# Performance work log

Measured on AMD Instinct MI355X. Metric: run time of the kernel, lower is better.

The kernel has to match this reference:

```python
import jax, jax.numpy as jnp
import numpy as np

B, C, OC, H, W = 2, 64, 128, 96, 96
HD, DI, N, R, K = C // 2, C, 16, 2, 4  # VSSBlock: hidden=C/2, d_inner=2*hidden=C, d_state, dt_rank, 4 scan dirs
EPS = 1e-5


def _conv(x, w, b, pad, groups=1):
    y = jax.lax.conv_general_dilated(x, w, (1, 1), pad, feature_group_count=groups,
                                     dimension_numbers=('NCHW', 'OIHW', 'NCHW'))
    return y + b[None, :, None, None]


def _ln(x, w, b):
    m = x.mean(-1, keepdims=True)
    v = x.var(-1, keepdims=True)
    return (x - m) * jax.lax.rsqrt(v + EPS) * w + b


def _selective_scan(xs, dts, Bs, Cs, A, D):
    # xs, dts: (B,K,DI,L); Bs, Cs: (B,K,N,L); A: (K,DI,N); D: (K,DI)
    dts = jax.nn.softplus(dts)

    def step(h, inp):
        u_t, dt_t, B_t, C_t = inp
        dA = jnp.exp(dt_t[..., None] * A)                         # (B,K,DI,N)
        h = dA * h + (dt_t * u_t)[..., None] * B_t[:, :, None, :]
        return h, jnp.einsum('bkdn,bkn->bkd', h, C_t)

    seq = (jnp.moveaxis(xs, -1, 0), jnp.moveaxis(dts, -1, 0),
           jnp.moveaxis(Bs, -1, 0), jnp.moveaxis(Cs, -1, 0))
    h0 = jnp.zeros(xs.shape[:3] + (A.shape[-1],), xs.dtype)
    _, ys = jax.lax.scan(step, h0, seq)
    return jnp.moveaxis(ys, 0, -1) + D[None, :, :, None] * xs


def _vss_block(x, ln_w, ln_b, in_w, conv_w, conv_b, xproj_w, dtproj_w, dtproj_b,
               A_logs, Ds, on_w, on_b, out_w):
    # x: (B,H,W,HD); VMamba SS2D with 4-direction cross-scan + residual
    b, hh, ww, _ = x.shape
    L = hh * ww
    h = _ln(x, ln_w, ln_b)
    xz = h @ in_w                                   # (B,H,W,2*DI)
    xp, z = jnp.split(xz, 2, axis=-1)
    xc = jnp.transpose(xp, (0, 3, 1, 2))            # (B,DI,H,W)
    xc = jax.nn.silu(_conv(xc, conv_w, conv_b, ((1, 1), (1, 1)), groups=DI))
    x_flat = xc.reshape(b, DI, L)
    x_wh = jnp.transpose(xc, (0, 1, 3, 2)).reshape(b, DI, L)
    x2 = jnp.stack([x_flat, x_wh], axis=1)
    xs = jnp.concatenate([x2, jnp.flip(x2, -1)], axis=1)      # (B,4,DI,L)
    x_dbl = jnp.einsum('bkdl,kcd->bkcl', xs, xproj_w)
    dts, Bs, Cs = jnp.split(x_dbl, [R, R + N], axis=2)
    dts = jnp.einsum('bkrl,kdr->bkdl', dts, dtproj_w) + dtproj_b[None, :, :, None]
    A = -jnp.exp(A_logs)
    ys = _selective_scan(xs, dts, Bs, Cs, A, Ds)              # (B,4,DI,L)
    inv = jnp.flip(ys[:, 2:4], -1)
    unwh = lambda t: jnp.transpose(t.reshape(b, DI, ww, hh), (0, 1, 3, 2)).reshape(b, DI, L)
    y = ys[:, 0] + inv[:, 0] + unwh(ys[:, 1]) + unwh(inv[:, 1])
    y = jnp.transpose(y.reshape(b, DI, hh, ww), (0, 2, 3, 1))
    y = _ln(y, on_w, on_b) * jax.nn.silu(z)
    return x + y @ out_w


def _forward(x, ms_dw33_w, ms_dw33_b, ms_in_w, ms_in_b, ms_scale,
             vss_ln_w, vss_ln_b, vss_in_w, vss_conv_w, vss_conv_b, vss_xproj_w,
             vss_dtproj_w, vss_dtproj_b, vss_A_logs, vss_Ds, vss_on_w, vss_on_b, vss_out_w,
             ma_conv_w, ma_conv_b, adw_h_w, adw_h_b, adw_w_w, adw_w_b,
             pw_w, pw_b, bn_w, bn_b, bn_mean, bn_var):
    vss = (vss_ln_w, vss_ln_b, vss_in_w, vss_conv_w, vss_conv_b, vss_xproj_w,
           vss_dtproj_w, vss_dtproj_b, vss_A_logs, vss_Ds, vss_on_w, vss_on_b, vss_out_w)
    # --- MambaSplit (shared VSSBlock applied to both channel halves) ---
    xd = _conv(x, ms_dw33_w, ms_dw33_b, ((1, 1), (1, 1)), groups=C)
    x1, x2 = jnp.split(xd, 2, axis=1)

    def branch(xp):
        y = _vss_block(jnp.transpose(xp, (0, 2, 3, 1)), *vss)
        return ms_scale * xp + jnp.transpose(y, (0, 3, 1, 2))

    xm = jnp.concatenate([branch(x1), branch(x2)], axis=1)
    m = xm.mean((2, 3), keepdims=True)
    v = xm.var((2, 3), keepdims=True)
    xm = (xm - m) * jax.lax.rsqrt(v + EPS) * ms_in_w[None, :, None, None] + ms_in_b[None, :, None, None]
    xm = jax.nn.leaky_relu(xm, 0.01)
    # --- MaxAvg (global avg+max pool -> 3x3 conv on 1x1 map -> sigmoid gate) ---
    pooled = jnp.concatenate([x.mean((2, 3), keepdims=True), x.max((2, 3), keepdims=True)], axis=1)
    gate = jax.nn.sigmoid(_conv(pooled, ma_conv_w, ma_conv_b, ((1, 1), (1, 1))))
    xs_ = xm + gate * x
    # --- AxialDW ---
    xs_ = xs_ + _conv(xs_, adw_h_w, adw_h_b, ((1, 1), (0, 0)), groups=C) \
              + _conv(xs_, adw_w_w, adw_w_b, ((0, 0), (1, 1)), groups=C)
    # --- BN (eval) + ReLU, 1x1 conv, 2x2 maxpool ---
    skip = jax.nn.relu((xs_ - bn_mean[None, :, None, None]) * jax.lax.rsqrt(bn_var[None, :, None, None] + EPS)
                       * bn_w[None, :, None, None] + bn_b[None, :, None, None])
    out = _conv(skip, pw_w, pw_b, ((0, 0), (0, 0)))
    down = jax.lax.reduce_window(out, -jnp.inf, jax.lax.max, (1, 1, 2, 2), (1, 1, 2, 2), 'VALID')
    return down, skip


def setup_inputs() -> dict:
    key = jax.random.key(0)
    ks = jax.random.split(key, 16)
    r = lambda i, shape, s=0.02: jax.random.normal(ks[i], shape, jnp.float32) * s
    return {
        'x': jax.random.normal(ks[0], (B, C, H, W), jnp.float32),
        'ms_dw33_w': r(1, (C, 1, 3, 3), 0.1), 'ms_dw33_b': jnp.zeros(C),
        'ms_in_w': jnp.ones(C), 'ms_in_b': jnp.zeros(C),
        'ms_scale': jnp.ones((1,)),
        'vss_ln_w': jnp.ones(HD), 'vss_ln_b': jnp.zeros(HD),
        'vss_in_w': r(2, (HD, 2 * DI)),
        'vss_conv_w': r(3, (DI, 1, 3, 3), 0.1), 'vss_conv_b': jnp.zeros(DI),
        'vss_xproj_w': r(4, (K, R + 2 * N, DI)),
        'vss_dtproj_w': r(5, (K, DI, R), 0.1), 'vss_dtproj_b': r(6, (K, DI), 0.1),
        'vss_A_logs': jnp.tile(jnp.log(jnp.arange(1, N + 1, dtype=jnp.float32)), (K, DI, 1)),
        'vss_Ds': jnp.ones((K, DI)),
        'vss_on_w': jnp.ones(DI), 'vss_on_b': jnp.zeros(DI),
        'vss_out_w': r(7, (DI, HD)),
        'ma_conv_w': r(8, (C, 2 * C, 3, 3), 0.05), 'ma_conv_b': jnp.zeros(C),
        'adw_h_w': r(9, (C, 1, 3, 1), 0.1), 'adw_h_b': jnp.zeros(C),
        'adw_w_w': r(10, (C, 1, 1, 3), 0.1), 'adw_w_b': jnp.zeros(C),
        'pw_w': r(11, (OC, C, 1, 1)), 'pw_b': jnp.zeros(OC),
        'bn_w': jnp.ones(C), 'bn_b': jnp.zeros(C),
        'bn_mean': jnp.zeros(C), 'bn_var': jnp.ones(C),
    }


def reference(x, ms_dw33_w, ms_dw33_b, ms_in_w, ms_in_b, ms_scale,
              vss_ln_w, vss_ln_b, vss_in_w, vss_conv_w, vss_conv_b, vss_xproj_w,
              vss_dtproj_w, vss_dtproj_b, vss_A_logs, vss_Ds, vss_on_w, vss_on_b, vss_out_w,
              ma_conv_w, ma_conv_b, adw_h_w, adw_h_b, adw_w_w, adw_w_b,
              pw_w, pw_b, bn_w, bn_b, bn_mean, bn_var):
    return _forward(x, ms_dw33_w, ms_dw33_b, ms_in_w, ms_in_b, ms_scale,
                    vss_ln_w, vss_ln_b, vss_in_w, vss_conv_w, vss_conv_b, vss_xproj_w,
                    vss_dtproj_w, vss_dtproj_b, vss_A_logs, vss_Ds, vss_on_w, vss_on_b, vss_out_w,
                    ma_conv_w, ma_conv_b, adw_h_w, adw_h_b, adw_w_w, adw_w_b,
                    pw_w, pw_b, bn_w, bn_b, bn_mean, bn_var)
```

## Files before the change

kernel.cpp:

```cpp
#include <hip/hip_runtime.h>
#include <hip/hip_bf16.h>

typedef __hip_bfloat16 bf16;
#define DEV __device__ __forceinline__

constexpr int B_ = 2, C_ = 64, H_ = 96, W_ = 96, L_ = 9216;
constexpr int HD_ = 32, DI_ = 64, N_ = 16, K_ = 4, BB_ = 4;
constexpr int OC_ = 128;
constexpr int CH_ = 384, CL_ = 24;
constexpr int SEGN = 32, SEGC = 12;
constexpr int BROW = 20;
constexpr float EPSF = 1e-5f;
constexpr int DOWN_SZ = B_ * OC_ * 48 * 48;

typedef __attribute__((ext_vector_type(8))) short short8;
typedef __attribute__((ext_vector_type(4))) float f32x4;
typedef __attribute__((ext_vector_type(2))) float f32x2;

DEV float softplusf(float x) { return x > 15.f ? x : __logf(1.f + __expf(x)); }
DEV float b2f(bf16 v) { return __bfloat162float(v); }
DEV float lo16f(unsigned v) { return __uint_as_float(v << 16); }
DEV float hi16f(unsigned v) { return __uint_as_float(v & 0xffff0000u); }
DEV f32x2 pk2(unsigned w) { f32x2 r = {lo16f(w), hi16f(w)}; return r; }
DEV f32x2 lo2(f32x4 q) { f32x2 r = {q.x, q.y}; return r; }
DEV f32x2 hi2(f32x4 q) { f32x2 r = {q.z, q.w}; return r; }
DEV unsigned pkbf(float a, float b) {
  __hip_bfloat162 t;
  t.x = __float2bfloat16(a);
  t.y = __float2bfloat16(b);
  return *reinterpret_cast<unsigned*>(&t);
}
DEV void unpk8(uint4 a, float* v) {
  v[0] = lo16f(a.x); v[1] = hi16f(a.x); v[2] = lo16f(a.y); v[3] = hi16f(a.y);
  v[4] = lo16f(a.z); v[5] = hi16f(a.z); v[6] = lo16f(a.w); v[7] = hi16f(a.w);
}
DEV void unpk(uint4 a, uint4 b, float* v) {
  unpk8(a, v); unpk8(b, v + 8);
}

__constant__ float kLogN[16] = {
  0.0f, 0.69314718f, 1.09861229f, 1.38629436f, 1.60943791f, 1.79175947f,
  1.94591015f, 2.07944154f, 2.19722458f, 2.30258509f, 2.39789527f,
  2.48490665f, 2.56494936f, 2.63905733f, 2.70805020f, 2.77258872f};

DEV void pow_tree2(float e1, f32x2* ep) {
  float e2 = e1 * e1;
  ep[0].x = e1; ep[0].y = e2;
  f32x2 b2v = {e2, e2};
  ep[1] = ep[0] * b2v;
  float e4 = ep[1].y;
  f32x2 b4v = {e4, e4};
  ep[2] = ep[0] * b4v;
  ep[3] = ep[1] * b4v;
  float e8 = ep[3].y;
  f32x2 b8v = {e8, e8};
  ep[4] = ep[0] * b8v;
  ep[5] = ep[1] * b8v;
  ep[6] = ep[2] * b8v;
  ep[7] = ep[3] * b8v;
}

__global__ __launch_bounds__(256, 4) void k_front(
    const float* __restrict__ x, const float* __restrict__ dw33w,
    const float* __restrict__ dw33b, const float* __restrict__ lnw,
    const float* __restrict__ lnb, const float* __restrict__ inw,
    const float* __restrict__ xpw, const float* __restrict__ alog,
    float* __restrict__ xd, bf16* __restrict__ xzAh, bf16* __restrict__ xzBh,
    bf16* __restrict__ wh, float* __restrict__ aux) {
  int bb = blockIdx.y, t = threadIdx.x;
  int b = bb & 1, co = (bb >> 1) * HD_;
  int idx0 = blockIdx.x * 32;
  if (bb == 0) {
    int i = blockIdx.x * 256 + t;
    if (i < 144 * 64) {
      int n = i >> 6;
      wh[i] = __float2bfloat16(n < 136 ? xpw[i] : 0.f);
    }
    if (blockIdx.x == 0) {
      int kd = t;
      const float* al = alog + kd * N_;
      float a0 = al[0];
      bool lin = true;
#pragma unroll
      for (int n = 1; n < N_; n++) lin = lin && (fabsf(al[n] - a0 - kLogN[n]) < 3e-5f);
      aux[kd] = -__expf(a0);
      aux[256 + kd] = lin ? 1.f : 0.f;
#pragma unroll
      for (int n = 0; n < N_; n++) aux[512 + kd * N_ + n] = -__expf(al[n]);
    }
  }
  __shared__ float xds[32 * 36];
  __shared__ float meanA[32], rstdA[32];
  for (int i = t; i < 1024; i += 256) {
    int cl = i >> 5, ii = i & 31;
    int sp = idx0 + ii, wi = sp % 96, hi = sp / 96;
    int cg = b * C_ + co + cl;
    float acc = dw33b[co + cl];
#pragma unroll
    for (int dy = -1; dy <= 1; dy++) {
      int hh = hi + dy; if (hh < 0 || hh >= H_) continue;
#pragma unroll
      for (int dx = -1; dx <= 1; dx++) {
        int ww = wi + dx; if (ww < 0 || ww >= W_) continue;
        acc = fmaf(x[(size_t)cg * L_ + sp + dy * 96 + dx],
                   dw33w[(co + cl) * 9 + (dy + 1) * 3 + (dx + 1)], acc);
      }
    }
    xds[cl * 36 + ii] = acc;
    xd[(size_t)cg * L_ + sp] = acc;
  }
  __syncthreads();
  if (t < 32) {
    float s = 0.f, sq = 0.f;
#pragma unroll
    for (int c = 0; c < 32; c++) { float v = xds[c * 36 + t]; s += v; sq = fmaf(v, v, sq); }
    float mean = s * (1.f / HD_);
    float var = sq * (1.f / HD_) - mean * mean;
    meanA[t] = mean; rstdA[t] = rsqrtf(var + EPSF);
  }
  __syncthreads();
  for (int i = t; i < 1024; i += 256) {
    int c = i >> 5, idx = i & 31;
    float v = xds[c * 36 + idx];
    xds[c * 36 + idx] = (v - meanA[idx]) * rstdA[idx] * lnw[c] + lnb[c];
  }
  __syncthreads();
  int oc = t & 127, g = t >> 7;
  float acc[16];
#pragma unroll
  for (int j = 0; j < 16; j++) acc[j] = 0.f;
  for (int c = 0; c < 32; c++) {
    float wv = inw[c * 128 + oc];
    const float4* row = reinterpret_cast<const float4*>(&xds[c * 36 + g * 16]);
#pragma unroll
    for (int j4 = 0; j4 < 4; j4++) {
      float4 xv = row[j4];
      acc[j4 * 4 + 0] = fmaf(xv.x, wv, acc[j4 * 4 + 0]);
      acc[j4 * 4 + 1] = fmaf(xv.y, wv, acc[j4 * 4 + 1]);
      acc[j4 * 4 + 2] = fmaf(xv.z, wv, acc[j4 * 4 + 2]);
      acc[j4 * 4 + 3] = fmaf(xv.w, wv, acc[j4 * 4 + 3]);
    }
  }
  int occ = oc & 63;
  if (oc < 64) {
#pragma unroll
    for (int j = 0; j < 16; j++)
      xzAh[(size_t)(bb * L_ + idx0 + g * 16 + j) * 64 + occ] = __float2bfloat16(acc[j]);
  } else {
#pragma unroll
    for (int j = 0; j < 16; j++)
      xzBh[(size_t)(bb * L_ + idx0 + g * 16 + j) * 64 + occ] = __float2bfloat16(acc[j]);
  }
}

__global__ void k_dwsilu(const bf16* __restrict__ xzAh, const float* __restrict__ cw,
                         const float* __restrict__ cb, bf16* __restrict__ xch,
                         bf16* __restrict__ xcht) {
  int t = blockIdx.x * 256 + threadIdx.x;
  int dp = t & 31, idx = (t >> 5) % L_, bb = t / (L_ * 32);
  int d0 = dp * 2;
  int wi = idx % W_, hi = idx / W_;
  const unsigned* src = (const unsigned*)xzAh;
  float acc0 = cb[d0], acc1 = cb[d0 + 1];
#pragma unroll
  for (int dy = -1; dy <= 1; dy++) {
    int hh = hi + dy; if (hh < 0 || hh >= H_) continue;
#pragma unroll
    for (int dx = -1; dx <= 1; dx++) {
      int ww = wi + dx; if (ww < 0 || ww >= W_) continue;
      unsigned v = src[(size_t)(bb * L_ + hh * W_ + ww) * 32 + dp];
      float w0 = cw[d0 * 9 + (dy + 1) * 3 + (dx + 1)];
      float w1 = cw[(d0 + 1) * 9 + (dy + 1) * 3 + (dx + 1)];
      acc0 = fmaf(lo16f(v), w0, acc0);
      acc1 = fmaf(hi16f(v), w1, acc1);
    }
  }
  acc0 = acc0 / (1.f + __expf(-acc0));
  acc1 = acc1 / (1.f + __expf(-acc1));
  unsigned out = pkbf(acc0, acc1);
  ((unsigned*)xch)[t] = out;
  int idx_t = wi * 96 + hi;
  ((unsigned*)xcht)[((size_t)bb * L_ + idx_t) * 32 + dp] = out;
}

__global__ __launch_bounds__(256, 4) void k_xdbl_mfma(
    const bf16* __restrict__ xch, const bf16* __restrict__ wh,
    float* __restrict__ xdblB, float* __restrict__ xdblC) {
  int w = threadIdx.x >> 6, lane = threadIdx.x & 63;
  int bb = blockIdx.y;
  int mtile = blockIdx.x * 4 + w;
  int idx0 = mtile * 16;
  int m = lane & 15, quad = lane >> 4;
  const bf16* arow = xch + ((size_t)bb * L_ + idx0 + m) * 64 + quad * 8;
  short8 a0 = *reinterpret_cast<const short8*>(arow);
  short8 a1 = *reinterpret_cast<const short8*>(arow + 32);
  int ntb = blockIdx.z * 3;
#pragma unroll
  for (int it = 0; it < 3; it++) {
    int nt = ntb + it;
    int n = nt * 16 + m;
    const bf16* brow = wh + n * 64 + quad * 8;
    short8 b0 = *reinterpret_cast<const short8*>(brow);
    short8 b1 = *reinterpret_cast<const short8*>(brow + 32);
    f32x4 acc = {0.f, 0.f, 0.f, 0.f};
    acc = __builtin_amdgcn_mfma_f32_16x16x32_bf16(a0, b0, acc, 0, 0, 0);
    acc = __builtin_amdgcn_mfma_f32_16x16x32_bf16(a1, b1, acc, 0, 0, 0);
    if (n < 136) {
      int k4 = (n >= 102) ? 3 : (n >= 68) ? 2 : (n >= 34) ? 1 : 0;
      int c = n - k4 * 34;
#pragma unroll
      for (int i = 0; i < 4; i++) {
        int r = idx0 + quad * 4 + i;
        int hi2 = r / 96, wi2 = r - hi2 * 96;
        int tr = wi2 * 96 + hi2;
        int ls = (k4 == 0) ? r : (k4 == 1) ? tr : (k4 == 2) ? (L_ - 1 - r) : (L_ - 1 - tr);
        size_t row = (size_t)(bb * K_ + k4) * L_ + ls;
        if (c < 2)       xdblB[row * BROW + 16 + c] = acc[i];
        else if (c < 18) xdblB[row * BROW + (c - 2)] = acc[i];
        else             xdblC[row * 16 + (c - 18)] = acc[i];
      }
    }
  }
}

__global__ __launch_bounds__(256, 4) void k_scan1(
    const float* __restrict__ xdblB, const bf16* __restrict__ xch,
    const bf16* __restrict__ xcht, const float* __restrict__ dtw,
    const float* __restrict__ dtb, const float* __restrict__ aux,
    bf16* __restrict__ hbuf, float* __restrict__ ssum) {
  int w = threadIdx.x >> 6, d = threadIdx.x & 63;
  int bx = blockIdx.x;
  int chunk = bx * 4 + w, k = blockIdx.y, bb = blockIdx.z;
  const float* bB = xdblB + (size_t)(bb * K_ + k) * L_ * BROW;
  __shared__ __align__(16) float sB[96 * BROW];
  {
    const uint4* src = (const uint4*)(bB + (size_t)bx * 96 * BROW);
    uint4* dst = (uint4*)sB;
    for (int i = threadIdx.x; i < 480; i += 256) dst[i] = src[i];
  }
  __syncthreads();
  float w0 = dtw[(k * DI_ + d) * 2 + 0], w1 = dtw[(k * DI_ + d) * 2 + 1];
  float bia = dtb[k * DI_ + d];
  float A1 = aux[k * 64 + d];
  bool chain = (__ballot(aux[256 + k * 64 + d] > 0.5f) == ~0ull);
  const bf16* ub = ((k & 1) ? xcht : xch) + (size_t)bb * L_ * DI_;
  int ls0 = chunk * CL_;
  int uidx0 = (k & 2) ? (L_ - 1 - ls0) : ls0;
  int ustep = (k & 2) ? -1 : 1;
  float S = 0.f;
  size_t base = (size_t)((bb * K_ + k) * CH_ + chunk) * DI_ + d;
  if (chain) {
    float uv[CL_];
    const bf16* up = ub + (size_t)uidx0 * DI_ + d;
#pragma unroll
    for (int s = 0; s < CL_; s++) uv[s] = b2f(up[s * ustep * DI_]);
    f32x2 h2[8];
#pragma unroll
    for (int i = 0; i < 8; i++) { h2[i].x = 0.f; h2[i].y = 0.f; }
#pragma unroll
    for (int s = 0; s < CL_; s++) {
      const float* p = sB + (w * CL_ + s) * BROW;
      f32x4 q0 = *(const f32x4*)p;
      f32x4 q1 = *(const f32x4*)(p + 4);
      f32x4 q2 = *(const f32x4*)(p + 8);
      f32x4 q3 = *(const f32x4*)(p + 12);
      f32x2 tt = *(const f32x2*)(p + 16);
      float dt = softplusf(fmaf(tt.x, w0, fmaf(tt.y, w1, bia)));
      S += dt;
      float du = dt * uv[s];
      f32x2 du2 = {du, du};
      f32x2 ep2[8];
      pow_tree2(__expf(dt * A1), ep2);
      h2[0] = ep2[0] * h2[0] + du2 * lo2(q0);
      h2[1] = ep2[1] * h2[1] + du2 * hi2(q0);
      h2[2] = ep2[2] * h2[2] + du2 * lo2(q1);
      h2[3] = ep2[3] * h2[3] + du2 * hi2(q1);
      h2[4] = ep2[4] * h2[4] + du2 * lo2(q2);
      h2[5] = ep2[5] * h2[5] + du2 * hi2(q2);
      h2[6] = ep2[6] * h2[6] + du2 * lo2(q3);
      h2[7] = ep2[7] * h2[7] + du2 * hi2(q3);
    }
    uint4 o0, o1;
    o0.x = pkbf(h2[0].x, h2[0].y); o0.y = pkbf(h2[1].x, h2[1].y);
    o0.z = pkbf(h2[2].x, h2[2].y); o0.w = pkbf(h2[3].x, h2[3].y);
    o1.x = pkbf(h2[4].x, h2[4].y); o1.y = pkbf(h2[5].x, h2[5].y);
    o1.z = pkbf(h2[6].x, h2[6].y); o1.w = pkbf(h2[7].x, h2[7].y);
    *(uint4*)(hbuf + base * N_) = o0;
    *(uint4*)(hbuf + base * N_ + 8) = o1;
  } else {
    float h[N_];
#pragma unroll
    for (int n = 0; n < N_; n++) h[n] = 0.f;
    float A[N_];
#pragma unroll
    for (int n = 0; n < N_; n++) A[n] = aux[512 + (k * 64 + d) * N_ + n];
    for (int s = 0; s < CL_; s++) {
      const float* p = sB + (w * CL_ + s) * BROW;
      float u = b2f(ub[(size_t)(uidx0 + s * ustep) * DI_ + d]);
      float dt = softplusf(fmaf(p[16], w0, fmaf(p[17], w1, bia)));
      S += dt;
      float du = dt * u;
#pragma unroll
      for (int n = 0; n < N_; n++) h[n] = fmaf(__expf(dt * A[n]), h[n], du * p[n]);
    }
#pragma unroll
    for (int n = 0; n < N_; n++) hbuf[base * N_ + n] = __float2bfloat16(h[n]);
  }
  ssum[base] = S;
}

__global__ __launch_bounds__(256, 4) void k_scan2a(
    const float* __restrict__ aux, const float* __restrict__ ssum,
    bf16* __restrict__ hbuf, float* __restrict__ cumS,
    float* __restrict__ segH, float* __restrict__ segS) {
  int t = blockIdx.x * 256 + threadIdx.x;
  int n = t & 15, d = (t >> 4) & 63, kk = (t >> 10) & 3, bb = (t >> 12) & 3, seg = t >> 14;
  float A = aux[512 + (kk * 64 + d) * N_ + n];
  size_t row = (size_t)(bb * K_ + kk) * CH_ * DI_ + d;
  float hp = 0.f, Sc = 0.f;
#pragma unroll 4
  for (int j = 0; j < SEGC; j++) {
    int c = seg * SEGC + j;
    size_t sb = row + (size_t)c * DI_;
    float S = ssum[sb];
    float hl = b2f(hbuf[sb * N_ + n]);
    hbuf[sb * N_ + n] = __float2bfloat16(hp);
    if (n == 0) cumS[sb] = Sc;
    hp = fmaf(__expf(A * S), hp, hl);
    Sc += S;
  }
  size_t sbase = (size_t)(bb * K_ + kk) * SEGN + seg;
  segH[(sbase * DI_ + d) * N_ + n] = hp;
  if (n == 0) segS[sbase * DI_ + d] = Sc;
}

__global__ void k_scan2b(const float* __restrict__ aux, float* __restrict__ segH,
                         const float* __restrict__ segS) {
  int t = blockIdx.x * 256 + threadIdx.x;
  int n = t & 15, d = (t >> 4) & 63, kk = (t >> 10) & 3, bb = t >> 12;
  float A = aux[512 + (kk * 64 + d) * N_ + n];
  float hp = 0.f;
  for (int seg = 0; seg < SEGN; seg++) {
    size_t sbase = (size_t)(bb * K_ + kk) * SEGN + seg;
    size_t si = (sbase * DI_ + d) * N_ + n;
    float H = segH[si];
    float E = __expf(A * segS[sbase * DI_ + d]);
    segH[si] = hp;
    hp = fmaf(E, hp, H);
  }
}

__global__ __launch_bounds__(256, 4) void k_scan3(
    const float* __restrict__ xdblB, const float* __restrict__ xdblC,
    const bf16* __restrict__ xch, const bf16* __restrict__ xcht,
    const float* __restrict__ dtw, const float* __restrict__ dtb,
    const float* __restrict__ Dsw, const float* __restrict__ aux,
    const bf16* __restrict__ hbuf, const float* __restrict__ cumS,
    const float* __restrict__ segH, bf16* __restrict__ ydir) {
  int w = threadIdx.x >> 6, d = threadIdx.x & 63;
  int bx = blockIdx.x;
  int chunk = bx * 4 + w, k = blockIdx.y, bb = blockIdx.z;
  const float* bB = xdblB + (size_t)(bb * K_ + k) * L_ * BROW;
  const float* bC = xdblC + (size_t)(bb * K_ + k) * L_ * 16;
  __shared__ __align__(16) float sB[96 * BROW];
  __shared__ __align__(16) float sC[96 * 16];
  {
    const uint4* srcB = (const uint4*)(bB + (size_t)bx * 96 * BROW);
    uint4* dstB = (uint4*)sB;
    for (int i = threadIdx.x; i < 480; i += 256) dstB[i] = srcB[i];
    const uint4* srcC = (const uint4*)(bC + (size_t)bx * 96 * 16);
    uint4* dstC = (uint4*)sC;
    for (int i = threadIdx.x; i < 384; i += 256) dstC[i] = srcC[i];
  }
  __syncthreads();
  float w0 = dtw[(k * DI_ + d) * 2 + 0], w1 = dtw[(k * DI_ + d) * 2 + 1];
  float bia = dtb[k * DI_ + d];
  float Dk = Dsw[k * DI_ + d];
  float A1 = aux[k * 64 + d];
  bool chain = (__ballot(aux[256 + k * 64 + d] > 0.5f) == ~0ull);
  size_t base = (size_t)((bb * K_ + k) * CH_ + chunk) * DI_ + d;
  int seg = chunk / SEGC;
  size_t sbase = (size_t)(bb * K_ + k) * SEGN + seg;
  float Sc = cumS[base];
  const bf16* ub = ((k & 1) ? xcht : xch) + (size_t)bb * L_ * DI_;
  bf16* yb = ydir + (size_t)(bb * K_ + k) * L_ * DI_;
  int ls0 = chunk * CL_;
  int uidx0 = (k & 2) ? (L_ - 1 - ls0) : ls0;
  int ustep = (k & 2) ? -1 : 1;
  const bf16* hb = hbuf + base * N_;
  const float* Hin = segH + (sbase * DI_ + d) * N_;
  if (chain) {
    float uv[CL_];
    const bf16* up = ub + (size_t)uidx0 * DI_ + d;
#pragma unroll
    for (int s = 0; s < CL_; s++) uv[s] = b2f(up[s * ustep * DI_]);
    f32x2 h2[8];
    {
      uint4 qh0 = *(const uint4*)hb, qh1 = *(const uint4*)(hb + 8);
      h2[0] = pk2(qh0.x); h2[1] = pk2(qh0.y); h2[2] = pk2(qh0.z); h2[3] = pk2(qh0.w);
      h2[4] = pk2(qh1.x); h2[5] = pk2(qh1.y); h2[6] = pk2(qh1.z); h2[7] = pk2(qh1.w);
      f32x2 ep2[8];
      pow_tree2(__expf(A1 * Sc), ep2);
#pragma unroll
      for (int i = 0; i < 8; i++)
        h2[i] = ep2[i] * (*(const f32x2*)(Hin + 2 * i)) + h2[i];
    }
#pragma unroll
    for (int s = 0; s < CL_; s++) {
      int lr = w * CL_ + s;
      const float* p = sB + lr * BROW;
      const float* pc = sC + lr * 16;
      f32x4 q0 = *(const f32x4*)p;
      f32x4 q1 = *(const f32x4*)(p + 4);
      f32x4 q2 = *(const f32x4*)(p + 8);
      f32x4 q3 = *(const f32x4*)(p + 12);
      f32x2 tt = *(const f32x2*)(p + 16);
      f32x4 c0 = *(const f32x4*)pc;
      f32x4 c1 = *(const f32x4*)(pc + 4);
      f32x4 c2 = *(const f32x4*)(pc + 8);
      f32x4 c3 = *(const f32x4*)(pc + 12);
      float dt = softplusf(fmaf(tt.x, w0, fmaf(tt.y, w1, bia)));
      float du = dt * uv[s];
      f32x2 du2 = {du, du};
      f32x2 ep2[8];
      pow_tree2(__expf(dt * A1), ep2);
      f32x2 y2 = {0.f, 0.f};
      h2[0] = ep2[0] * h2[0] + du2 * lo2(q0);  y2 = h2[0] * lo2(c0) + y2;
      h2[1] = ep2[1] * h2[1] + du2 * hi2(q0);  y2 = h2[1] * hi2(c0) + y2;
      h2[2] = ep2[2] * h2[2] + du2 * lo2(q1);  y2 = h2[2] * lo2(c1) + y2;
      h2[3] = ep2[3] * h2[3] + du2 * hi2(q1);  y2 = h2[3] * hi2(c1) + y2;
      h2[4] = ep2[4] * h2[4] + du2 * lo2(q2);  y2 = h2[4] * lo2(c2) + y2;
      h2[5] = ep2[5] * h2[5] + du2 * hi2(q2);  y2 = h2[5] * hi2(c2) + y2;
      h2[6] = ep2[6] * h2[6] + du2 * lo2(q3);  y2 = h2[6] * lo2(c3) + y2;
      h2[7] = ep2[7] * h2[7] + du2 * hi2(q3);  y2 = h2[7] * hi2(c3) + y2;
      float y = fmaf(Dk, uv[s], y2.x + y2.y);
      yb[(size_t)(ls0 + s) * DI_ + d] = __float2bfloat16(y);
    }
  } else {
    float h[N_];
    {
      uint4 qh0 = *(const uint4*)hb, qh1 = *(const uint4*)(hb + 8);
      unpk(qh0, qh1, h);
#pragma unroll
      for (int n = 0; n < N_; n++) {
        float A = aux[512 + (k * 64 + d) * N_ + n];
        h[n] = fmaf(__expf(A * Sc), Hin[n], h[n]);
      }
    }
    float A[N_];
#pragma unroll
    for (int n = 0; n < N_; n++) A[n] = aux[512 + (k * 64 + d) * N_ + n];
    for (int s = 0; s < CL_; s++) {
      int lr = w * CL_ + s;
      const float* p = sB + lr * BROW;
      const float* pc = sC + lr * 16;
      float u = b2f(ub[(size_t)(uidx0 + s * ustep) * DI_ + d]);
      float dt = softplusf(fmaf(p[16], w0, fmaf(p[17], w1, bia)));
      float du = dt * u;
      float y = 0.f;
#pragma unroll
      for (int n = 0; n < N_; n++) {
        h[n] = fmaf(__expf(dt * A[n]), h[n], du * p[n]);
        y = fmaf(h[n], pc[n], y);
      }
      y = fmaf(Dk, u, y);
      yb[(size_t)(ls0 + s) * DI_ + d] = __float2bfloat16(y);
    }
  }
}

__global__ void k_combine(const bf16* __restrict__ ydir, const bf16* __restrict__ xzBh,
                          const float* __restrict__ xd, const float* __restrict__ onw,
                          const float* __restrict__ onb, const float* __restrict__ outw,
                          const float* __restrict__ mssc, float* __restrict__ xm) {
  int w = threadIdx.x >> 6, d = threadIdx.x & 63;
  int idx = blockIdx.x * 4 + w, bb = blockIdx.y;
  int b = bb & 1, co = (bb >> 1) * HD_;
  int hii = idx / 96, wii = idx - hii * 96;
  int lt = wii * 96 + hii;
  const bf16* yd = ydir + (size_t)bb * K_ * L_ * DI_;
  float y = b2f(yd[((size_t)0 * L_ + idx) * DI_ + d])
          + b2f(yd[((size_t)1 * L_ + lt) * DI_ + d])
          + b2f(yd[((size_t)2 * L_ + (L_ - 1 - idx)) * DI_ + d])
          + b2f(yd[((size_t)3 * L_ + (L_ - 1 - lt)) * DI_ + d]);
  float s = y, sq = y * y;
#pragma unroll
  for (int m = 1; m < 64; m <<= 1) { s += __shfl_xor(s, m, 64); sq += __shfl_xor(sq, m, 64); }
  float mean = s * (1.f / DI_);
  float var = sq * (1.f / DI_) - mean * mean;
  float rstd = rsqrtf(var + EPSF);
  float yn = (y - mean) * rstd * onw[d] + onb[d];
  float z = b2f(xzBh[(size_t)(bb * L_ + idx) * 64 + d]);
  float g = yn * (z / (1.f + __expf(-z)));
  __shared__ __align__(16) float gs[4][DI_];
  gs[w][d] = g;
  __syncthreads();
  int dh = d & 31;
  int ddb = (d >= 32) ? 32 : 0;
  const float* grow = &gs[w][ddb];
  float acc = 0.f;
#pragma unroll
  for (int j = 0; j < 8; j++) {
    float4 gv = *(const float4*)(grow + j * 4);
    int dd = ddb + j * 4;
    acc = fmaf(gv.x, outw[(dd + 0) * HD_ + dh], acc);
    acc = fmaf(gv.y, outw[(dd + 1) * HD_ + dh], acc);
    acc = fmaf(gv.z, outw[(dd + 2) * HD_ + dh], acc);
    acc = fmaf(gv.w, outw[(dd + 3) * HD_ + dh], acc);
  }
  acc += __shfl_xor(acc, 32, 64);
  if (d < HD_) {
    size_t xi = (size_t)(b * C_ + co + d) * L_ + idx;
    float xp = xd[xi];
    xm[xi] = mssc[0] * xp + xp + acc;
  }
}

__global__ __launch_bounds__(1024) void k_stats(
    const float* __restrict__ xm, const float* __restrict__ x,
    float* __restrict__ inm, float* __restrict__ inr,
    float* __restrict__ xmean, float* __restrict__ xmax) {
  int bc = blockIdx.x, t = threadIdx.x;
  const float4* pm4 = (const float4*)(xm + (size_t)bc * L_);
  const float4* px4 = (const float4*)(x + (size_t)bc * L_);
  float s = 0.f, sq = 0.f, xs = 0.f, mx = -1e30f;
  for (int i = t; i < L_ / 4; i += 1024) {
    float4 v = pm4[i];
    s += (v.x + v.y) + (v.z + v.w);
    sq = fmaf(v.x, v.x, sq); sq = fmaf(v.y, v.y, sq);
    sq = fmaf(v.z, v.z, sq); sq = fmaf(v.w, v.w, sq);
    float4 xv = px4[i];
    xs += (xv.x + xv.y) + (xv.z + xv.w);
    mx = fmaxf(mx, fmaxf(fmaxf(xv.x, xv.y), fmaxf(xv.z, xv.w)));
  }
  __shared__ float red[64];
#pragma unroll
  for (int m = 1; m < 64; m <<= 1) {
    s += __shfl_xor(s, m, 64); sq += __shfl_xor(sq, m, 64);
    xs += __shfl_xor(xs, m, 64); mx = fmaxf(mx, __shfl_xor(mx, m, 64));
  }
  int wid = t >> 6;
  if ((t & 63) == 0) { red[wid] = s; red[16 + wid] = sq; red[32 + wid] = xs; red[48 + wid] = mx; }
  __syncthreads();
  if (t == 0) {
    s = 0.f; sq = 0.f; xs = 0.f; mx = -1e30f;
#pragma unroll
    for (int i = 0; i < 16; i++) {
      s += red[i]; sq += red[16 + i]; xs += red[32 + i]; mx = fmaxf(mx, red[48 + i]);
    }
    float mean = s * (1.f / L_);
    float var = sq * (1.f / L_) - mean * mean;
    inm[bc] = mean;
    inr[bc] = rsqrtf(var + EPSF);
    xmean[bc] = xs * (1.f / L_);
    xmax[bc] = mx;
  }
}

__global__ void k_axbn(const float* __restrict__ xm, const float* __restrict__ x,
                       const float* __restrict__ inm, const float* __restrict__ inr,
                       const float* __restrict__ msw, const float* __restrict__ msb,
                       const float* __restrict__ xmean, const float* __restrict__ xmax,
                       const float* __restrict__ maw, const float* __restrict__ mab,
                       const float* __restrict__ hw, const float* __restrict__ hb,
                       const float* __restrict__ wwt, const float* __restrict__ wb,
                       const float* __restrict__ bnw, const float* __restrict__ bnb,
                       const float* __restrict__ bnm, const float* __restrict__ bnv,
                       float* __restrict__ skipo) {
  constexpr int NEL = B_ * C_ * L_;
  int t0 = blockIdx.x * 256;
  int t = t0 + threadIdx.x;
  int bc = t0 / L_, c = bc & 63, b = bc >> 6;
  __shared__ float gsh;
  __shared__ float sxs[448];
  if (threadIdx.x < 64) {
    int ic = threadIdx.x;
    float p = xmean[b * 64 + ic] * maw[(c * 128 + ic) * 9 + 4]
            + xmax[b * 64 + ic] * maw[(c * 128 + 64 + ic) * 9 + 4];
#pragma unroll
    for (int m = 1; m < 64; m <<= 1) p += __shfl_xor(p, m, 64);
    if (ic == 0) gsh = 1.f / (1.f + __expf(-(p + mab[c])));
  }
  __syncthreads();
  float gate = gsh, im = inm[bc], ir = inr[bc], mw = msw[c], mb = msb[c];
  for (int i = threadIdx.x; i < 448; i += 256) {
    int tt = t0 - 96 + i;
    tt = tt < 0 ? 0 : (tt >= NEL ? NEL - 1 : tt);
    float v = xm[tt];
    v = (v - im) * ir * mw + mb;
    v = v > 0.f ? v : 0.01f * v;
    sxs[i] = v + gate * x[tt];
  }
  __syncthreads();
  int li = 96 + threadIdx.x;
  int wi = t % W_, hi = (t / W_) % H_;
  float a = sxs[li];
  float hacc = hb[c];
#pragma unroll
  for (int dy = -1; dy <= 1; dy++) {
    int hh = hi + dy; if (hh < 0 || hh >= H_) continue;
    hacc = fmaf(sxs[li + dy * 96], hw[c * 3 + dy + 1], hacc);
  }
  float wacc = wb[c];
#pragma unroll
  for (int dx = -1; dx <= 1; dx++) {
    int ww = wi + dx; if (ww < 0 || ww >= W_) continue;
    wacc = fmaf(sxs[li + dx], wwt[c * 3 + dx + 1], wacc);
  }
  float v = a + hacc + wacc;
  float sv = (v - bnm[c]) * rsqrtf(bnv[c] + EPSF) * bnw[c] + bnb[c];
  skipo[t] = fmaxf(sv, 0.f);
}

__global__ void k_pwpool(const float* __restrict__ skipo, const float* __restrict__ pww,
                         const float* __restrict__ pwb, float* __restrict__ down) {
  int h2 = blockIdx.x, b = blockIdx.y, t = threadIdx.x;
  int oc0 = blockIdx.z * 32;
  __shared__ __align__(8) float sk[64 * 192];
  for (int i = t; i < 64 * 192; i += 256) {
    int c = i / 192, rw = i % 192, r = rw / 96, wcol = rw % 96;
    sk[i] = skipo[((size_t)(b * C_ + c) * H_ + (2 * h2 + r)) * W_ + wcol];
  }
  __syncthreads();
  for (int o = t; o < 32 * 48; o += 256) {
    int oc = oc0 + o / 48, w2 = o % 48;
    float s0 = 0.f, s1 = 0.f, s2 = 0.f, s3 = 0.f;
#pragma unroll 8
    for (int c = 0; c < 64; c++) {
      float wv = pww[oc * 64 + c];
      const float2* sp = (const float2*)&sk[c * 192 + 2 * w2];
      float2 r0 = sp[0];
      float2 r1 = sp[48];
      s0 = fmaf(r0.x, wv, s0);
      s1 = fmaf(r0.y, wv, s1);
      s2 = fmaf(r1.x, wv, s2);
      s3 = fmaf(r1.y, wv, s3);
    }
    float v = fmaxf(fmaxf(s0, s1), fmaxf(s2, s3)) + pwb[oc];
    down[((size_t)(b * OC_ + oc) * 48 + h2) * 48 + w2] = v;
  }
}

extern "C" void kernel_launch(void* const* d_in, const int* in_sizes, int n_in,
                              void* d_out, int out_size, void* d_ws, size_t ws_size,
                              hipStream_t stream) {
  const float* x     = (const float*)d_in[0];
  const float* dw33w = (const float*)d_in[1];
  const float* dw33b = (const float*)d_in[2];
  const float* msw   = (const float*)d_in[3];
  const float* msb   = (const float*)d_in[4];
  const float* mssc  = (const float*)d_in[5];
  const float* lnw   = (const float*)d_in[6];
  const float* lnb   = (const float*)d_in[7];
  const float* inw   = (const float*)d_in[8];
  const float* cw    = (const float*)d_in[9];
  const float* cb    = (const float*)d_in[10];
  const float* xpw   = (const float*)d_in[11];
  const float* dtw   = (const float*)d_in[12];
  const float* dtb   = (const float*)d_in[13];
  const float* alog  = (const float*)d_in[14];
  const float* Dsw   = (const float*)d_in[15];
  const float* onw   = (const float*)d_in[16];
  const float* onb   = (const float*)d_in[17];
  const float* outw  = (const float*)d_in[18];
  const float* maw   = (const float*)d_in[19];
  const float* mab   = (const float*)d_in[20];
  const float* ahw   = (const float*)d_in[21];
  const float* ahb   = (const float*)d_in[22];
  const float* aww   = (const float*)d_in[23];
  const float* awb   = (const float*)d_in[24];
  const float* pww   = (const float*)d_in[25];
  const float* pwb   = (const float*)d_in[26];
  const float* bnw   = (const float*)d_in[27];
  const float* bnb   = (const float*)d_in[28];
  const float* bnm   = (const float*)d_in[29];
  const float* bnv   = (const float*)d_in[30];

  float* ws = (float*)d_ws;
  float* xd    = ws;
  float* hreg  = xd + 1179648;
  bf16*  hbuf  = (bf16*)hreg;
  bf16*  xzAh  = (bf16*)hreg;
  bf16*  xzBh  = (bf16*)(hreg + 1179648);
  float* xdblB = hreg + 1179648 + 1179648;
  float* xdblC = xdblB + 2949120;
  float* ssum  = xdblC + 2359296;
  bf16*  ydir  = (bf16*)(ssum + 393216);
  float* xmR   = ssum + 393216 + 4718592;
  bf16*  xch   = (bf16*)xmR;
  float* xm    = xmR;
  float* st    = xmR + 1179648;
  float* inm = st, *inr = st + 128, *xmean = st + 256, *xmaxv = st + 384;
  float* aux   = st + 512;
  bf16*  wh    = (bf16*)(aux + 4608);
  float* cumS  = aux + 4608 + 4608;
  float* segH  = cumS + 393216;
  float* segS  = segH + 524288;
  bf16*  xcht  = (bf16*)(segS + 32768);

  float* outp = (float*)d_out;
  float* down = outp;
  float* skipo = outp + DOWN_SZ;

  dim3 b256(256);
  int nEl = B_ * C_ * L_;

  k_front<<<dim3(L_ / 32, BB_), b256, 0, stream>>>(x, dw33w, dw33b, lnw, lnb, inw,
                                                   xpw, alog, xd, xzAh, xzBh, wh, aux);
  k_dwsilu<<<dim3(BB_ * L_ * 32 / 256), b256, 0, stream>>>(xzAh, cw, cb, xch, xcht);
  k_xdbl_mfma<<<dim3(L_ / 64, BB_, 3), b256, 0, stream>>>(xch, wh, xdblB, xdblC);
  k_scan1<<<dim3(CH_ / 4, K_, BB_), b256, 0, stream>>>(xdblB, xch, xcht, dtw, dtb, aux, hbuf, ssum);
  k_scan2a<<<dim3(BB_ * K_ * SEGN * DI_ * N_ / 256), b256, 0, stream>>>(aux, ssum, hbuf, cumS, segH, segS);
  k_scan2b<<<dim3(BB_ * K_ * DI_ * N_ / 256), b256, 0, stream>>>(aux, segH, segS);
  k_scan3<<<dim3(CH_ / 4, K_, BB_), b256, 0, stream>>>(xdblB, xdblC, xch, xcht, dtw, dtb, Dsw,
                                                      aux, hbuf, cumS, segH, ydir);
  k_combine<<<dim3(L_ / 4, BB_), b256, 0, stream>>>(ydir, xzBh, xd, onw, onb, outw, mssc, xm);
  k_stats<<<dim3(B_ * C_), dim3(1024), 0, stream>>>(xm, x, inm, inr, xmean, xmaxv);
  k_axbn<<<dim3((nEl + 255) / 256), b256, 0, stream>>>(xm, x, inm, inr, msw, msb, xmean, xmaxv,
                                                      maw, mab, ahw, ahb, aww, awb,
                                                      bnw, bnb, bnm, bnv, skipo);
  k_pwpool<<<dim3(48, B_, 4), b256, 0, stream>>>(skipo, pww, pwb, down);
}
```

Before: 286.1 us.

## Fuse depthwise conv into x_proj MFMA and fold channel stats into producers

Merges the depthwise conv+SiLU kernel with the x_proj MFMA kernel, so the conv output tile is kept in shared memory and fed straight into the MFMA instead of being re-read from global memory. Removes the separate stats kernel: the mean and max of x are reduced with atomics in k_front, and the sum and sum-of-squares of xm are accumulated with atomics in k_combine, with a memset up front to zero them. This saves two launches and one full pass over xm and x. In exchange there are many atomic operations, run-to-run float nondeterminism, and a variance computed as E[x^2]-mean^2 from atomic sums.

After: 407.4 us. 42.4% more time.

```diff
diff --git a/kernel.cpp b/kernel.cpp
--- a/kernel.cpp
+++ b/kernel.cpp
@@ -36,6 +36,14 @@
 }
 DEV void unpk(uint4 a, uint4 b, float* v) {
   unpk8(a, v); unpk8(b, v + 8);
+}
+DEV unsigned encmax(float f) {
+  unsigned u = __float_as_uint(f);
+  return (u & 0x80000000u) ? ~u : (u | 0x80000000u);
+}
+DEV float decmax(unsigned k) {
+  unsigned u = (k & 0x80000000u) ? (k & 0x7fffffffu) : ~k;
+  return __uint_as_float(u);
 }
 
 __constant__ float kLogN[16] = {
@@ -66,7 +74,8 @@
     const float* __restrict__ lnb, const float* __restrict__ inw,
     const float* __restrict__ xpw, const float* __restrict__ alog,
     float* __restrict__ xd, bf16* __restrict__ xzAh, bf16* __restrict__ xzBh,
-    bf16* __restrict__ wh, float* __restrict__ aux) {
+    bf16* __restrict__ wh, float* __restrict__ aux,
+    float* __restrict__ xsum, unsigned* __restrict__ xmk) {
   int bb = blockIdx.y, t = threadIdx.x;
   int b = bb & 1, co = (bb >> 1) * HD_;
   int idx0 = blockIdx.x * 32;
@@ -108,6 +117,17 @@
     }
     xds[cl * 36 + ii] = acc;
     xd[(size_t)cg * L_ + sp] = acc;
+    float xr = x[(size_t)cg * L_ + sp];
+    float xs = xr, xmx = xr;
+#pragma unroll
+    for (int m2 = 1; m2 < 32; m2 <<= 1) {
+      xs += __shfl_xor(xs, m2, 64);
+      xmx = fmaxf(xmx, __shfl_xor(xmx, m2, 64));
+    }
+    if ((t & 31) == 0) {
+      atomicAdd(&xsum[cg], xs);
+      atomicMax(&xmk[cg], encmax(xmx));
+    }
   }
   __syncthreads();
   if (t < 32) {
@@ -153,51 +173,50 @@
   }
 }
 
-__global__ void k_dwsilu(const bf16* __restrict__ xzAh, const float* __restrict__ cw,
-                         const float* __restrict__ cb, bf16* __restrict__ xch,
-                         bf16* __restrict__ xcht) {
-  int t = blockIdx.x * 256 + threadIdx.x;
-  int dp = t & 31, idx = (t >> 5) % L_, bb = t / (L_ * 32);
-  int d0 = dp * 2;
-  int wi = idx % W_, hi = idx / W_;
+__global__ __launch_bounds__(256, 4) void k_dwx(
+    const bf16* __restrict__ xzAh, const float* __restrict__ cw,
+    const float* __restrict__ cb, const bf16* __restrict__ wh,
+    bf16* __restrict__ xch, bf16* __restrict__ xcht,
+    float* __restrict__ xdblB, float* __restrict__ xdblC) {
+  int idx0 = blockIdx.x * 64, bb = blockIdx.y;
+  int t = threadIdx.x;
+  __shared__ __align__(16) bf16 sA[64 * 64];
   const unsigned* src = (const unsigned*)xzAh;
-  float acc0 = cb[d0], acc1 = cb[d0 + 1];
-#pragma unroll
-  for (int dy = -1; dy <= 1; dy++) {
-    int hh = hi + dy; if (hh < 0 || hh >= H_) continue;
-#pragma unroll
-    for (int dx = -1; dx <= 1; dx++) {
-      int ww = wi + dx; if (ww < 0 || ww >= W_) continue;
-      unsigned v = src[(size_t)(bb * L_ + hh * W_ + ww) * 32 + dp];
-      float w0 = cw[d0 * 9 + (dy + 1) * 3 + (dx + 1)];
-      float w1 = cw[(d0 + 1) * 9 + (dy + 1) * 3 + (dx + 1)];
-      acc0 = fmaf(lo16f(v), w0, acc0);
-      acc1 = fmaf(hi16f(v), w1, acc1);
-    }
-  }
-  acc0 = acc0 / (1.f + __expf(-acc0));
-  acc1 = acc1 / (1.f + __expf(-acc1));
-  unsigned out = pkbf(acc0, acc1);
-  ((unsigned*)xch)[t] = out;
-  int idx_t = wi * 96 + hi;
-  ((unsigned*)xcht)[((size_t)bb * L_ + idx_t) * 32 + dp] = out;
-}
-
-__global__ __launch_bounds__(256, 4) void k_xdbl_mfma(
-    const bf16* __restrict__ xch, const bf16* __restrict__ wh,
-    float* __restrict__ xdblB, float* __restrict__ xdblC) {
-  int w = threadIdx.x >> 6, lane = threadIdx.x & 63;
-  int bb = blockIdx.y;
-  int mtile = blockIdx.x * 4 + w;
-  int idx0 = mtile * 16;
+  unsigned* sAu = (unsigned*)sA;
+  for (int item = t; item < 2048; item += 256) {
+    int li = item >> 5, dp = item & 31;
+    int idx = idx0 + li;
+    int wi = idx % W_, hi = idx / W_;
+    int d0 = dp * 2;
+    float acc0 = cb[d0], acc1 = cb[d0 + 1];
+#pragma unroll
+    for (int dy = -1; dy <= 1; dy++) {
+      int hh = hi + dy; if (hh < 0 || hh >= H_) continue;
+#pragma unroll
+      for (int dx = -1; dx <= 1; dx++) {
+        int ww = wi + dx; if (ww < 0 || ww >= W_) continue;
+        unsigned v = src[(size_t)(bb * L_ + hh * W_ + ww) * 32 + dp];
+        acc0 = fmaf(lo16f(v), cw[d0 * 9 + (dy + 1) * 3 + (dx + 1)], acc0);
+        acc1 = fmaf(hi16f(v), cw[(d0 + 1) * 9 + (dy + 1) * 3 + (dx + 1)], acc1);
+      }
+    }
+    acc0 = acc0 / (1.f + __expf(-acc0));
+    acc1 = acc1 / (1.f + __expf(-acc1));
+    unsigned out = pkbf(acc0, acc1);
+    sAu[li * 32 + dp] = out;
+    ((unsigned*)xch)[((size_t)bb * L_ + idx) * 32 + dp] = out;
+    int idx_t = wi * 96 + hi;
+    ((unsigned*)xcht)[((size_t)bb * L_ + idx_t) * 32 + dp] = out;
+  }
+  __syncthreads();
+  int w = t >> 6, lane = t & 63;
   int m = lane & 15, quad = lane >> 4;
-  const bf16* arow = xch + ((size_t)bb * L_ + idx0 + m) * 64 + quad * 8;
+  const bf16* arow = sA + (w * 16 + m) * 64 + quad * 8;
   short8 a0 = *reinterpret_cast<const short8*>(arow);
   short8 a1 = *reinterpret_cast<const short8*>(arow + 32);
-  int ntb = blockIdx.z * 3;
-#pragma unroll
-  for (int it = 0; it < 3; it++) {
-    int nt = ntb + it;
+  int midx0 = idx0 + w * 16;
+#pragma unroll
+  for (int nt = 0; nt < 9; nt++) {
     int n = nt * 16 + m;
     const bf16* brow = wh + n * 64 + quad * 8;
     short8 b0 = *reinterpret_cast<const short8*>(brow);
@@ -210,7 +229,7 @@
       int c = n - k4 * 34;
 #pragma unroll
       for (int i = 0; i < 4; i++) {
-        int r = idx0 + quad * 4 + i;
+        int r = midx0 + quad * 4 + i;
         int hi2 = r / 96, wi2 = r - hi2 * 96;
         int tr = wi2 * 96 + hi2;
         int ls = (k4 == 0) ? r : (k4 == 1) ? tr : (k4 == 2) ? (L_ - 1 - r) : (L_ - 1 - tr);
@@ -472,7 +491,8 @@
 __global__ void k_combine(const bf16* __restrict__ ydir, const bf16* __restrict__ xzBh,
                           const float* __restrict__ xd, const float* __restrict__ onw,
                           const float* __restrict__ onb, const float* __restrict__ outw,
-                          const float* __restrict__ mssc, float* __restrict__ xm) {
+                          const float* __restrict__ mssc, float* __restrict__ xm,
+                          float* __restrict__ s1, float* __restrict__ s2) {
   int w = threadIdx.x >> 6, d = threadIdx.x & 63;
   int idx = blockIdx.x * 4 + w, bb = blockIdx.y;
   int b = bb & 1, co = (bb >> 1) * HD_;
@@ -509,58 +529,27 @@
     acc = fmaf(gv.w, outw[(dd + 3) * HD_ + dh], acc);
   }
   acc += __shfl_xor(acc, 32, 64);
+  __shared__ float vs[4][32], vq[4][32];
   if (d < HD_) {
     size_t xi = (size_t)(b * C_ + co + d) * L_ + idx;
     float xp = xd[xi];
-    xm[xi] = mssc[0] * xp + xp + acc;
-  }
-}
-
-__global__ __launch_bounds__(1024) void k_stats(
-    const float* __restrict__ xm, const float* __restrict__ x,
-    float* __restrict__ inm, float* __restrict__ inr,
-    float* __restrict__ xmean, float* __restrict__ xmax) {
-  int bc = blockIdx.x, t = threadIdx.x;
-  const float4* pm4 = (const float4*)(xm + (size_t)bc * L_);
-  const float4* px4 = (const float4*)(x + (size_t)bc * L_);
-  float s = 0.f, sq = 0.f, xs = 0.f, mx = -1e30f;
-  for (int i = t; i < L_ / 4; i += 1024) {
-    float4 v = pm4[i];
-    s += (v.x + v.y) + (v.z + v.w);
-    sq = fmaf(v.x, v.x, sq); sq = fmaf(v.y, v.y, sq);
-    sq = fmaf(v.z, v.z, sq); sq = fmaf(v.w, v.w, sq);
-    float4 xv = px4[i];
-    xs += (xv.x + xv.y) + (xv.z + xv.w);
-    mx = fmaxf(mx, fmaxf(fmaxf(xv.x, xv.y), fmaxf(xv.z, xv.w)));
-  }
-  __shared__ float red[64];
-#pragma unroll
-  for (int m = 1; m < 64; m <<= 1) {
-    s += __shfl_xor(s, m, 64); sq += __shfl_xor(sq, m, 64);
-    xs += __shfl_xor(xs, m, 64); mx = fmaxf(mx, __shfl_xor(mx, m, 64));
-  }
-  int wid = t >> 6;
-  if ((t & 63) == 0) { red[wid] = s; red[16 + wid] = sq; red[32 + wid] = xs; red[48 + wid] = mx; }
-  __syncthreads();
-  if (t == 0) {
-    s = 0.f; sq = 0.f; xs = 0.f; mx = -1e30f;
-#pragma unroll
-    for (int i = 0; i < 16; i++) {
-      s += red[i]; sq += red[16 + i]; xs += red[32 + i]; mx = fmaxf(mx, red[48 + i]);
-    }
-    float mean = s * (1.f / L_);
-    float var = sq * (1.f / L_) - mean * mean;
-    inm[bc] = mean;
-    inr[bc] = rsqrtf(var + EPSF);
-    xmean[bc] = xs * (1.f / L_);
-    xmax[bc] = mx;
+    float v = mssc[0] * xp + xp + acc;
+    xm[xi] = v;
+    vs[w][d] = v; vq[w][d] = v * v;
+  }
+  __syncthreads();
+  if (threadIdx.x < 32) {
+    int dd = threadIdx.x;
+    float a1 = (vs[0][dd] + vs[1][dd]) + (vs[2][dd] + vs[3][dd]);
+    float a2 = (vq[0][dd] + vq[1][dd]) + (vq[2][dd] + vq[3][dd]);
+    atomicAdd(&s1[b * C_ + co + dd], a1);
+    atomicAdd(&s2[b * C_ + co + dd], a2);
   }
 }
 
 __global__ void k_axbn(const float* __restrict__ xm, const float* __restrict__ x,
-                       const float* __restrict__ inm, const float* __restrict__ inr,
+                       const float* __restrict__ stats,
                        const float* __restrict__ msw, const float* __restrict__ msb,
-                       const float* __restrict__ xmean, const float* __restrict__ xmax,
                        const float* __restrict__ maw, const float* __restrict__ mab,
                        const float* __restrict__ hw, const float* __restrict__ hb,
                        const float* __restrict__ wwt, const float* __restrict__ wb,
@@ -575,14 +564,18 @@
   __shared__ float sxs[448];
   if (threadIdx.x < 64) {
     int ic = threadIdx.x;
-    float p = xmean[b * 64 + ic] * maw[(c * 128 + ic) * 9 + 4]
-            + xmax[b * 64 + ic] * maw[(c * 128 + 64 + ic) * 9 + 4];
+    float xmv = stats[256 + b * 64 + ic] * (1.f / L_);
+    float xmx = decmax(((const unsigned*)stats)[384 + b * 64 + ic]);
+    float p = xmv * maw[(c * 128 + ic) * 9 + 4]
+            + xmx * maw[(c * 128 + 64 + ic) * 9 + 4];
 #pragma unroll
     for (int m = 1; m < 64; m <<= 1) p += __shfl_xor(p, m, 64);
     if (ic == 0) gsh = 1.f / (1.f + __expf(-(p + mab[c])));
   }
   __syncthreads();
-  float gate = gsh, im = inm[bc], ir = inr[bc], mw = msw[c], mb = msb[c];
+  float im = stats[bc] * (1.f / L_);
+  float ir = rsqrtf(stats[128 + bc] * (1.f / L_) - im * im + EPSF);
+  float gate = gsh, mw = msw[c], mb = msb[c];
   for (int i = threadIdx.x; i < 448; i += 256) {
     int tt = t0 - 96 + i;
     tt = tt < 0 ? 0 : (tt >= NEL ? NEL - 1 : tt);
@@ -690,7 +683,6 @@
   bf16*  xch   = (bf16*)xmR;
   float* xm    = xmR;
   float* st    = xmR + 1179648;
-  float* inm = st, *inr = st + 128, *xmean = st + 256, *xmaxv = st + 384;
   float* aux   = st + 512;
   bf16*  wh    = (bf16*)(aux + 4608);
   float* cumS  = aux + 4608 + 4608;
@@ -705,18 +697,19 @@
   dim3 b256(256);
   int nEl = B_ * C_ * L_;
 
+  hipMemsetAsync(st, 0, 512 * sizeof(float), stream);
   k_front<<<dim3(L_ / 32, BB_), b256, 0, stream>>>(x, dw33w, dw33b, lnw, lnb, inw,
-                                                   xpw, alog, xd, xzAh, xzBh, wh, aux);
-  k_dwsilu<<<dim3(BB_ * L_ * 32 / 256), b256, 0, stream>>>(xzAh, cw, cb, xch, xcht);
-  k_xdbl_mfma<<<dim3(L_ / 64, BB_, 3), b256, 0, stream>>>(xch, wh, xdblB, xdblC);
+                                                   xpw, alog, xd, xzAh, xzBh, wh, aux,
+                                                   st + 256, (unsigned*)(st + 384));
+  k_dwx<<<dim3(L_ / 64, BB_), b256, 0, stream>>>(xzAh, cw, cb, wh, xch, xcht, xdblB, xdblC);
   k_scan1<<<dim3(CH_ / 4, K_, BB_), b256, 0, stream>>>(xdblB, xch, xcht, dtw, dtb, aux, hbuf, ssum);
   k_scan2a<<<dim3(BB_ * K_ * SEGN * DI_ * N_ / 256), b256, 0, stream>>>(aux, ssum, hbuf, cumS, segH, segS);
   k_scan2b<<<dim3(BB_ * K_ * DI_ * N_ / 256), b256, 0, stream>>>(aux, segH, segS);
   k_scan3<<<dim3(CH_ / 4, K_, BB_), b256, 0, stream>>>(xdblB, xdblC, xch, xcht, dtw, dtb, Dsw,
                                                       aux, hbuf, cumS, segH, ydir);
-  k_combine<<<dim3(L_ / 4, BB_), b256, 0, stream>>>(ydir, xzBh, xd, onw, onb, outw, mssc, xm);
-  k_stats<<<dim3(B_ * C_), dim3(1024), 0, stream>>>(xm, x, inm, inr, xmean, xmaxv);
-  k_axbn<<<dim3((nEl + 255) / 256), b256, 0, stream>>>(xm, x, inm, inr, msw, msb, xmean, xmaxv,
+  k_combine<<<dim3(L_ / 4, BB_), b256, 0, stream>>>(ydir, xzBh, xd, onw, onb, outw, mssc, xm,
+                                                    st, st + 128);
+  k_axbn<<<dim3((nEl + 255) / 256), b256, 0, stream>>>(xm, x, st, msw, msb,
                                                       maw, mab, ahw, ahb, aww, awb,
                                                       bnw, bnb, bnm, bnv, skipo);
   k_pwpool<<<dim3(48, B_, 4), b256, 0, stream>>>(skipo, pww, pwb, down);
```
